# Performance work log

Hardware: AMD Instinct MI355X
Metric: run time of the kernel (lower is better)

## Reference

```python
import jax, jax.numpy as jnp
import numpy as np

B, G, CIN, COUT = 1024, 64, 512, 512  # G = s**(num_layers-1) = 2**6


def setup_inputs() -> dict:
    key = jax.random.key(0)
    kx, kw = jax.random.split(key)
    x = jax.random.normal(kx, (B, G, CIN), dtype=jnp.float32)
    weight = jax.random.normal(kw, (G, CIN, COUT), dtype=jnp.float32)
    return {"x": x, "weight": weight}


def reference(x, weight):
    # Original: (x[:,:,:,None] * W[None]).sum(2) / sqrt(Cin), then sum over groups.
    # Fused equivalent: grouped contraction over (g, c) -> [B, Cout].
    scale = 1.0 / jnp.sqrt(jnp.asarray(x.shape[2], dtype=x.dtype))
    out = jnp.einsum("bgc,gco->bo", x, weight) * scale
    return out
```

## Files before the change

### kernel.cpp

```cpp
#include <hip/hip_runtime.h>
#include <hip/hip_bf16.h>

typedef __bf16 bf16x8 __attribute__((ext_vector_type(8)));
typedef __bf16 bf16x4 __attribute__((ext_vector_type(4)));
typedef float  f32x4  __attribute__((ext_vector_type(4)));

#define B_SZ    1024
#define COUT_SZ 512
#define K_SZ    32768
#define TM 128
#define TN 128
#define BK 32
#define APITCH 36

__device__ __forceinline__ void async_copy16(const void* g, void* l) {
  __builtin_amdgcn_global_load_lds(
      (const __attribute__((address_space(1))) unsigned int*)g,
      (__attribute__((address_space(3))) unsigned int*)l, 16, 0, 0);
}

__global__ __launch_bounds__(256) void wtrans_kernel(
    const float* __restrict__ w, __bf16* __restrict__ wt) {
  __shared__ float t[64 * 65];
  const int kb = (blockIdx.x & 511) * 64;
  const int ob = (blockIdx.x >> 9) * 64;
  const int tid = threadIdx.x;
  {
    const int o4 = (tid & 15) * 4;
    const int kr = tid >> 4;
    const float* src = w + (size_t)(kb + kr) * COUT_SZ + ob + o4;
#pragma unroll
    for (int i = 0; i < 4; ++i) {
      f32x4 v = *(const f32x4*)(src + (size_t)(16 * i) * COUT_SZ);
      *(f32x4*)&t[(kr + 16 * i) * 65 + o4] = v;
    }
  }
  __syncthreads();
  {
    const int k4 = (tid & 15) * 4;
    const int orow = tid >> 4;
#pragma unroll
    for (int j = 0; j < 4; ++j) {
      const int o = orow + 16 * j;
      bf16x4 p;
#pragma unroll
      for (int e = 0; e < 4; ++e) p[e] = (__bf16)t[(k4 + e) * 65 + o];
      *(bf16x4*)(wt + (size_t)(ob + o) * K_SZ + kb + k4) = p;
    }
  }
}

__global__ __launch_bounds__(256, 4)
void gemm_kernel(const float* __restrict__ x, const __bf16* __restrict__ wt,
                 __bf16* __restrict__ dst, int kchunk, int S) {
  __shared__ __bf16 As[TM * APITCH];
  __shared__ __bf16 Bs[TN * BK];

  const int lin = blockIdx.x;
  const int z = lin % S;
  const int t = lin / S;
  const int m0 = (t & 7) * TM;
  const int n0 = (t >> 3) * TN;
  const int tid  = threadIdx.x;
  const int w    = tid >> 6;
  const int lane = tid & 63;
  const int kbase = z * kchunk;

  const int ar = tid >> 1;
  const int ah = tid & 1;
  const float* ag = x + (size_t)(m0 + ar) * K_SZ + kbase + ah * 16;
  __bf16* aw = &As[ar * APITCH + ah * 16];

  const int sRow = lane >> 2;
  const int sCh  = (lane & 3) ^ (sRow & 3);
  const __bf16* bg0 = wt + (size_t)(n0 + w * 32 + sRow) * K_SZ + kbase + sCh * 8;
  const __bf16* bg1 = wt + (size_t)(n0 + w * 32 + 16 + sRow) * K_SZ + kbase + sCh * 8;
  __bf16* bL0 = &Bs[(w * 32) * BK];
  __bf16* bL1 = &Bs[(w * 32 + 16) * BK];

  const int lm = lane & 15;
  const int q  = lane >> 4;
  const int wm = (w & 1) * 64;
  const int wn = (w >> 1) * 64;
  const int pc = q ^ (lm & 3);

  f32x4 acc[4][4];
#pragma unroll
  for (int i = 0; i < 4; ++i)
#pragma unroll
    for (int j = 0; j < 4; ++j)
      acc[i][j] = (f32x4){0.f, 0.f, 0.f, 0.f};

  const int niter = kchunk / BK;
  for (int it = 0; it < niter; ++it) {
    async_copy16(bg0, bL0);
    async_copy16(bg1, bL1);
    bg0 += BK; bg1 += BK;
    {
      f32x4 p0 = *(const f32x4*)(ag);
      f32x4 p1 = *(const f32x4*)(ag + 4);
      f32x4 p2 = *(const f32x4*)(ag + 8);
      f32x4 p3 = *(const f32x4*)(ag + 12);
      ag += BK;
      bf16x4 c0, c1, c2, c3;
#pragma unroll
      for (int e = 0; e < 4; ++e) {
        c0[e] = (__bf16)p0[e]; c1[e] = (__bf16)p1[e];
        c2[e] = (__bf16)p2[e]; c3[e] = (__bf16)p3[e];
      }
      *(bf16x4*)(aw)      = c0;
      *(bf16x4*)(aw + 4)  = c1;
      *(bf16x4*)(aw + 8)  = c2;
      *(bf16x4*)(aw + 12) = c3;
    }
    __syncthreads();

    bf16x8 af[4], bfr[4];
#pragma unroll
    for (int i = 0; i < 4; ++i) {
      const __bf16* arow = &As[(wm + i * 16 + lm) * APITCH + q * 8];
      bf16x4 lo = *(const bf16x4*)arow;
      bf16x4 hi = *(const bf16x4*)(arow + 4);
      bf16x8 a;
#pragma unroll
      for (int e = 0; e < 4; ++e) { a[e] = lo[e]; a[e + 4] = hi[e]; }
      af[i] = a;
    }
#pragma unroll
    for (int j = 0; j < 4; ++j)
      bfr[j] = *(const bf16x8*)&Bs[(wn + j * 16 + lm) * BK + pc * 8];

#pragma unroll
    for (int i = 0; i < 4; ++i)
#pragma unroll
      for (int j = 0; j < 4; ++j)
        acc[i][j] = __builtin_amdgcn_mfma_f32_16x16x32_bf16(af[i], bfr[j], acc[i][j], 0, 0, 0);

    __syncthreads();
  }

  __bf16* outp = dst + (size_t)z * (B_SZ * COUT_SZ)
               + (size_t)(m0 + wm + q * 4) * COUT_SZ + (n0 + wn + lm);
#pragma unroll
  for (int i = 0; i < 4; ++i) {
#pragma unroll
    for (int r = 0; r < 4; ++r) {
      __bf16* o2 = outp + (size_t)(i * 16 + r) * COUT_SZ;
#pragma unroll
      for (int j = 0; j < 4; ++j)
        o2[j * 16] = (__bf16)acc[i][j][r];
    }
  }
}

__global__ __launch_bounds__(256) void reduce_kernel(
    const __bf16* __restrict__ p, float* __restrict__ out, int S, float scale) {
  const size_t i = ((size_t)blockIdx.x * 256 + threadIdx.x) * 8;
  float s[8];
#pragma unroll
  for (int e = 0; e < 8; ++e) s[e] = 0.f;
  for (int zz = 0; zz < S; ++zz) {
    bf16x8 v = *(const bf16x8*)(p + (size_t)zz * (B_SZ * COUT_SZ) + i);
#pragma unroll
    for (int e = 0; e < 8; ++e) s[e] += (float)v[e];
  }
  f32x4 o0, o1;
#pragma unroll
  for (int e = 0; e < 4; ++e) { o0[e] = s[e] * scale; o1[e] = s[e + 4] * scale; }
  *(f32x4*)(out + i) = o0;
  *(f32x4*)(out + i + 4) = o1;
}

extern "C" void kernel_launch(void* const* d_in, const int* in_sizes, int n_in,
                              void* d_out, int out_size, void* d_ws, size_t ws_size,
                              hipStream_t stream) {
  const float* x = (const float*)d_in[0];
  const float* w = (const float*)d_in[1];
  float* out = (float*)d_out;

  const size_t wtB    = (size_t)COUT_SZ * K_SZ * sizeof(__bf16);
  const size_t sliceB = (size_t)B_SZ * COUT_SZ * sizeof(__bf16);

  __bf16* wt = (__bf16*)d_ws;
  __bf16* partials = (__bf16*)((char*)d_ws + wtB);

  int S = 32;
  while (S > 1 && wtB + (size_t)S * sliceB > ws_size) S >>= 1;

  const float scale = 0.04419417382415922f;

  hipLaunchKernelGGL(wtrans_kernel, dim3((K_SZ / 64) * (COUT_SZ / 64)), dim3(256),
                     0, stream, w, wt);
  hipLaunchKernelGGL(gemm_kernel, dim3(32 * S), dim3(256), 0, stream,
                     x, wt, partials, K_SZ / S, S);
  hipLaunchKernelGGL(reduce_kernel, dim3(B_SZ * COUT_SZ / (256 * 8)), dim3(256),
                     0, stream, partials, out, S, scale);
}
```

Before: 297.4 us.

## Drop LDS staging in split-K GEMM, load MFMA fragments directly from global

The GEMM kernel no longer stages A and B tiles through shared memory with barriers. Each lane now loads its MFMA fragments straight from global memory, converting x from fp32 to bf16 in registers. The block tile changes from 128x128 to 64x256: all four waves share the same 64 rows of A and each takes its own 64 columns of B. This removes the LDS traffic and both __syncthreads per iteration. In exchange, every wave loads the same A rows again from global or cache, and each lane's loads stride across rows, so accesses are less coalesced.

```diff
diff --git a/kernel.cpp b/kernel.cpp
--- a/kernel.cpp
+++ b/kernel.cpp
@@ -8,16 +8,7 @@
 #define B_SZ    1024
 #define COUT_SZ 512
 #define K_SZ    32768
-#define TM 128
-#define TN 128
 #define BK 32
-#define APITCH 36
-
-__device__ __forceinline__ void async_copy16(const void* g, void* l) {
-  __builtin_amdgcn_global_load_lds(
-      (const __attribute__((address_space(1))) unsigned int*)g,
-      (__attribute__((address_space(3))) unsigned int*)l, 16, 0, 0);
-}
 
 __global__ __launch_bounds__(256) void wtrans_kernel(
     const float* __restrict__ w, __bf16* __restrict__ wt) {
@@ -53,36 +44,26 @@
 __global__ __launch_bounds__(256, 4)
 void gemm_kernel(const float* __restrict__ x, const __bf16* __restrict__ wt,
                  __bf16* __restrict__ dst, int kchunk, int S) {
-  __shared__ __bf16 As[TM * APITCH];
-  __shared__ __bf16 Bs[TN * BK];
-
   const int lin = blockIdx.x;
   const int z = lin % S;
   const int t = lin / S;
-  const int m0 = (t & 7) * TM;
-  const int n0 = (t >> 3) * TN;
-  const int tid  = threadIdx.x;
-  const int w    = tid >> 6;
-  const int lane = tid & 63;
+  const int m0 = (t & 15) * 64;
+  const int n0 = (t >> 4) * 256;
+  const int w    = (threadIdx.x >> 6);
+  const int lane = threadIdx.x & 63;
+  const int lm = lane & 15;
+  const int q  = lane >> 4;
   const int kbase = z * kchunk;
 
-  const int ar = tid >> 1;
-  const int ah = tid & 1;
-  const float* ag = x + (size_t)(m0 + ar) * K_SZ + kbase + ah * 16;
-  __bf16* aw = &As[ar * APITCH + ah * 16];
-
-  const int sRow = lane >> 2;
-  const int sCh  = (lane & 3) ^ (sRow & 3);
-  const __bf16* bg0 = wt + (size_t)(n0 + w * 32 + sRow) * K_SZ + kbase + sCh * 8;
-  const __bf16* bg1 = wt + (size_t)(n0 + w * 32 + 16 + sRow) * K_SZ + kbase + sCh * 8;
-  __bf16* bL0 = &Bs[(w * 32) * BK];
-  __bf16* bL1 = &Bs[(w * 32 + 16) * BK];
-
-  const int lm = lane & 15;
-  const int q  = lane >> 4;
-  const int wm = (w & 1) * 64;
-  const int wn = (w >> 1) * 64;
-  const int pc = q ^ (lm & 3);
+  const float* ap0 = x + (size_t)(m0 + 0 * 16 + lm) * K_SZ + kbase + q * 8;
+  const float* ap1 = x + (size_t)(m0 + 1 * 16 + lm) * K_SZ + kbase + q * 8;
+  const float* ap2 = x + (size_t)(m0 + 2 * 16 + lm) * K_SZ + kbase + q * 8;
+  const float* ap3 = x + (size_t)(m0 + 3 * 16 + lm) * K_SZ + kbase + q * 8;
+  const int nb = n0 + w * 64;
+  const __bf16* bp0 = wt + (size_t)(nb + 0 * 16 + lm) * K_SZ + kbase + q * 8;
+  const __bf16* bp1 = wt + (size_t)(nb + 1 * 16 + lm) * K_SZ + kbase + q * 8;
+  const __bf16* bp2 = wt + (size_t)(nb + 2 * 16 + lm) * K_SZ + kbase + q * 8;
+  const __bf16* bp3 = wt + (size_t)(nb + 3 * 16 + lm) * K_SZ + kbase + q * 8;
 
   f32x4 acc[4][4];
 #pragma unroll
@@ -93,54 +74,37 @@
 
   const int niter = kchunk / BK;
   for (int it = 0; it < niter; ++it) {
-    async_copy16(bg0, bL0);
-    async_copy16(bg1, bL1);
-    bg0 += BK; bg1 += BK;
-    {
-      f32x4 p0 = *(const f32x4*)(ag);
-      f32x4 p1 = *(const f32x4*)(ag + 4);
-      f32x4 p2 = *(const f32x4*)(ag + 8);
-      f32x4 p3 = *(const f32x4*)(ag + 12);
-      ag += BK;
-      bf16x4 c0, c1, c2, c3;
+    f32x4 al0 = *(const f32x4*)ap0, ah0 = *(const f32x4*)(ap0 + 4);
+    f32x4 al1 = *(const f32x4*)ap1, ah1 = *(const f32x4*)(ap1 + 4);
+    f32x4 al2 = *(const f32x4*)ap2, ah2 = *(const f32x4*)(ap2 + 4);
+    f32x4 al3 = *(const f32x4*)ap3, ah3 = *(const f32x4*)(ap3 + 4);
+    bf16x8 bv0 = *(const bf16x8*)bp0;
+    bf16x8 bv1 = *(const bf16x8*)bp1;
+    bf16x8 bv2 = *(const bf16x8*)bp2;
+    bf16x8 bv3 = *(const bf16x8*)bp3;
+    ap0 += BK; ap1 += BK; ap2 += BK; ap3 += BK;
+    bp0 += BK; bp1 += BK; bp2 += BK; bp3 += BK;
+
+    bf16x8 av[4];
 #pragma unroll
-      for (int e = 0; e < 4; ++e) {
-        c0[e] = (__bf16)p0[e]; c1[e] = (__bf16)p1[e];
-        c2[e] = (__bf16)p2[e]; c3[e] = (__bf16)p3[e];
-      }
-      *(bf16x4*)(aw)      = c0;
-      *(bf16x4*)(aw + 4)  = c1;
-      *(bf16x4*)(aw + 8)  = c2;
-      *(bf16x4*)(aw + 12) = c3;
+    for (int e = 0; e < 4; ++e) {
+      av[0][e] = (__bf16)al0[e]; av[0][e + 4] = (__bf16)ah0[e];
+      av[1][e] = (__bf16)al1[e]; av[1][e + 4] = (__bf16)ah1[e];
+      av[2][e] = (__bf16)al2[e]; av[2][e + 4] = (__bf16)ah2[e];
+      av[3][e] = (__bf16)al3[e]; av[3][e + 4] = (__bf16)ah3[e];
     }
-    __syncthreads();
 
-    bf16x8 af[4], bfr[4];
 #pragma unroll
     for (int i = 0; i < 4; ++i) {
-      const __bf16* arow = &As[(wm + i * 16 + lm) * APITCH + q * 8];
-      bf16x4 lo = *(const bf16x4*)arow;
-      bf16x4 hi = *(const bf16x4*)(arow + 4);
-      bf16x8 a;
-#pragma unroll
-      for (int e = 0; e < 4; ++e) { a[e] = lo[e]; a[e + 4] = hi[e]; }
-      af[i] = a;
+      acc[i][0] = __builtin_amdgcn_mfma_f32_16x16x32_bf16(av[i], bv0, acc[i][0], 0, 0, 0);
+      acc[i][1] = __builtin_amdgcn_mfma_f32_16x16x32_bf16(av[i], bv1, acc[i][1], 0, 0, 0);
+      acc[i][2] = __builtin_amdgcn_mfma_f32_16x16x32_bf16(av[i], bv2, acc[i][2], 0, 0, 0);
+      acc[i][3] = __builtin_amdgcn_mfma_f32_16x16x32_bf16(av[i], bv3, acc[i][3], 0, 0, 0);
     }
-#pragma unroll
-    for (int j = 0; j < 4; ++j)
-      bfr[j] = *(const bf16x8*)&Bs[(wn + j * 16 + lm) * BK + pc * 8];
-
-#pragma unroll
-    for (int i = 0; i < 4; ++i)
-#pragma unroll
-      for (int j = 0; j < 4; ++j)
-        acc[i][j] = __builtin_amdgcn_mfma_f32_16x16x32_bf16(af[i], bfr[j], acc[i][j], 0, 0, 0);
-
-    __syncthreads();
   }
 
   __bf16* outp = dst + (size_t)z * (B_SZ * COUT_SZ)
-               + (size_t)(m0 + wm + q * 4) * COUT_SZ + (n0 + wn + lm);
+               + (size_t)(m0 + q * 4) * COUT_SZ + (nb + lm);
 #pragma unroll
   for (int i = 0; i < 4; ++i) {
 #pragma unroll
```

Result: slower. 388.8 us (+30.8%).
